# Kernel tuning notes

Hardware: AMD Instinct MI355X
Metric: run time of the kernel (lower is better)

## Reference

```python
import jax, jax.numpy as jnp
import numpy as np

N = 100000   # nodes
M = 50000    # hyperedges
E = 600000   # incidences
D_IN = 128
D_OUT = 128


def setup_inputs() -> dict:
    key = jax.random.key(0)
    ks = jax.random.split(key, 7)
    x = jax.random.normal(ks[0], (N, D_IN), dtype=jnp.float32)
    row = jax.random.randint(ks[1], (E,), 0, N, dtype=jnp.int64)  # node ids
    col = jax.random.randint(ks[2], (E,), 0, M, dtype=jnp.int64)  # hyperedge ids
    edge_index = jnp.stack([row, col], axis=0)
    s_v = 1.0 / np.sqrt(D_IN)
    s_e = 1.0 / np.sqrt(D_OUT)
    s_u = 1.0 / np.sqrt(2 * D_OUT)
    W_v = jax.random.uniform(ks[3], (D_IN, D_OUT), jnp.float32, -s_v, s_v)
    W_e = jax.random.uniform(ks[4], (D_OUT, D_OUT), jnp.float32, -s_e, s_e)
    W_upd = jax.random.uniform(ks[5], (2 * D_OUT, D_OUT), jnp.float32, -s_u, s_u)
    b_upd = jax.random.uniform(ks[6], (D_OUT,), jnp.float32, -s_u, s_u)
    return {"x": x, "edge_index": edge_index, "W_v": W_v, "W_e": W_e,
            "W_upd": W_upd, "b_upd": b_upd}


def _mean_reduce(vals, index, K):
    # vals: (E, D); scatter-mean into (K, D)
    s = jax.ops.segment_sum(vals, index, num_segments=K)
    cnt = jax.ops.segment_sum(jnp.ones((vals.shape[0], 1), vals.dtype), index,
                              num_segments=K)
    return s / jnp.maximum(cnt, 1.0)


def reference(x, edge_index, W_v, W_e, W_upd, b_upd):
    row, col = edge_index[0], edge_index[1]
    x_self = x @ W_v                                # (N, D)
    # vertex -> hyperedge (mean pooling)
    e_feat = _mean_reduce(x_self[row], col, M)      # (M, D)
    e_proj = e_feat @ W_e                           # (M, D)
    # hyperedge -> vertex (mean pooling)
    n_agg = _mean_reduce(e_proj[col], row, N)       # (N, D)
    out = jnp.concatenate([x_self, n_agg], axis=-1) # (N, 2D)
    return jax.nn.relu(out @ W_upd + b_upd)
```

## Files before the change

kernel.cpp:

```cpp
#include <hip/hip_runtime.h>

typedef unsigned short u16;
typedef unsigned int u32;
typedef __attribute__((ext_vector_type(8))) short bf16x8;
typedef __attribute__((ext_vector_type(4))) float f32x4;

__device__ inline u16 f2bf(float f) {
    u32 u = __float_as_uint(f);
    return (u16)((u + 0x7FFFu + ((u >> 16) & 1u)) >> 16);
}
__device__ inline bf16x8 pack8(float4 a, float4 b) {
    bf16x8 v = { (short)f2bf(a.x), (short)f2bf(a.y), (short)f2bf(a.z), (short)f2bf(a.w),
                 (short)f2bf(b.x), (short)f2bf(b.y), (short)f2bf(b.z), (short)f2bf(b.w) };
    return v;
}
__device__ inline float bflo(u32 v) { return __uint_as_float(v << 16); }
__device__ inline float bfhi(u32 v) { return __uint_as_float(v & 0xFFFF0000u); }

#define LDA 136
#define CAPE 64
#define CAPN 48
#define PE   6250
#define PN   12500

__device__ inline void gemm128_nolds(
    const float* __restrict__ A, const float* __restrict__ B, int tile,
    u16* __restrict__ Wt, int koff, float* __restrict__ Cf32)
{
    const int tid = threadIdx.x;
    const int col = tid & 127;
    const int rh  = tid >> 7;
    const int r0  = tile * 16;
    float acc[8] = {0.f,0.f,0.f,0.f,0.f,0.f,0.f,0.f};
    for (int k = 0; k < 128; ++k) {
        float bv = B[(size_t)k * 128 + col];
        #pragma unroll
        for (int i = 0; i < 8; ++i)
            acc[i] = fmaf(A[(size_t)(r0 + rh * 8 + i) * 128 + k], bv, acc[i]);
    }
    #pragma unroll
    for (int i = 0; i < 8; ++i) {
        int r = r0 + rh * 8 + i;
        if (Wt)   Wt[(size_t)col * 256 + koff + r] = f2bf(acc[i]);
        if (Cf32) Cf32[(size_t)r * 128 + col] = acc[i];
    }
}

__global__ __launch_bounds__(256) void fill_conv(
    const int* __restrict__ row, const int* __restrict__ col,
    int* __restrict__ cnt_e, int* __restrict__ cnt_n,
    int* __restrict__ adj_e, u16* __restrict__ adj_n, int E,
    const float* __restrict__ x, u16* __restrict__ xb, size_t n8, int nbConv,
    const float* __restrict__ W_v, const float* __restrict__ W_e,
    const float* __restrict__ W_upd, float* __restrict__ T,
    u16* __restrict__ Wt)
{
    u32 bid = blockIdx.x;
    if (bid < 16) {
        if (bid < 8) gemm128_nolds(W_v, W_upd, bid, Wt, 0, nullptr);
        else         gemm128_nolds(W_e, W_upd + 128 * 128, bid - 8, nullptr, 0, T);
        return;
    }
    bid -= 16;
    if (bid < (u32)nbConv) {
        size_t i = (size_t)bid * 256 + threadIdx.x;
        if (i < n8) {
            const float4* s = (const float4*)(x + i * 8);
            *(bf16x8*)(xb + i * 8) = pack8(s[0], s[1]);
        }
        return;
    }
    bid -= nbConv;
    const int chunk = bid >> 3;
    const int part  = bid & 7;
    const int e = chunk * 256 + threadIdx.x;
    if (e >= E) return;
    const int r = row[e], c = col[e];
    if ((u32)c / PE == (u32)part) {
        int pe = atomicAdd(&cnt_e[c], 1);
        if (pe < CAPE) adj_e[(size_t)c * CAPE + pe] = r;
    }
    if ((u32)r / PN == (u32)part) {
        int pn = atomicAdd(&cnt_n[r], 1);
        if (pn < CAPN) adj_n[(size_t)r * CAPN + pn] = (u16)c;
    }
}

template<typename IDX, int CAP>
__device__ inline void gather2_body(
    const u32* __restrict__ src, const IDX* __restrict__ adj,
    const int* __restrict__ cnt, u32* __restrict__ out, int K, int rowBase)
{
    const int tid = threadIdx.x;
    const int row = rowBase + ((tid >> 6) << 1) + ((tid & 63) >> 5);
    const int l32 = tid & 31;
    if (row >= K) return;
    int d = cnt[row];
    if (d > CAP) d = CAP;
    const IDX* a = adj + (size_t)row * CAP;
    float sA0=0.f,sA1=0.f,sA2=0.f,sA3=0.f;
    float sB0=0.f,sB1=0.f,sB2=0.f,sB3=0.f;
    int k = 0;
    for (; k + 4 <= d; k += 4) {
        uint2 v0 = *(const uint2*)(src + (size_t)(u32)a[k]     * 64 + l32 * 2);
        uint2 v1 = *(const uint2*)(src + (size_t)(u32)a[k + 1] * 64 + l32 * 2);
        uint2 v2 = *(const uint2*)(src + (size_t)(u32)a[k + 2] * 64 + l32 * 2);
        uint2 v3 = *(const uint2*)(src + (size_t)(u32)a[k + 3] * 64 + l32 * 2);
        sA0 += bflo(v0.x); sA1 += bfhi(v0.x); sA2 += bflo(v0.y); sA3 += bfhi(v0.y);
        sB0 += bflo(v1.x); sB1 += bfhi(v1.x); sB2 += bflo(v1.y); sB3 += bfhi(v1.y);
        sA0 += bflo(v2.x); sA1 += bfhi(v2.x); sA2 += bflo(v2.y); sA3 += bfhi(v2.y);
        sB0 += bflo(v3.x); sB1 += bfhi(v3.x); sB2 += bflo(v3.y); sB3 += bfhi(v3.y);
    }
    for (; k < d; ++k) {
        uint2 v = *(const uint2*)(src + (size_t)(u32)a[k] * 64 + l32 * 2);
        sA0 += bflo(v.x); sA1 += bfhi(v.x); sA2 += bflo(v.y); sA3 += bfhi(v.y);
    }
    float inv = 1.f / fmaxf((float)d, 1.f);
    float s0 = (sA0 + sB0) * inv, s1 = (sA1 + sB1) * inv;
    float s2 = (sA2 + sB2) * inv, s3 = (sA3 + sB3) * inv;
    uint2 res;
    res.x = ((u32)f2bf(s1) << 16) | (u32)f2bf(s0);
    res.y = ((u32)f2bf(s3) << 16) | (u32)f2bf(s2);
    *(uint2*)(out + (size_t)row * 64 + l32 * 2) = res;
}

__global__ __launch_bounds__(256) void gather_e_k(
    const u32* __restrict__ src, const int* __restrict__ adj,
    const int* __restrict__ cnt, u32* __restrict__ out, int K,
    const float* __restrict__ W_v, const float* __restrict__ T,
    u16* __restrict__ Wt)
{
    if (blockIdx.x < 8) {
        gemm128_nolds(W_v, T, blockIdx.x, Wt, 128, nullptr);
        return;
    }
    gather2_body<int, CAPE>(src, adj, cnt, out, K, (blockIdx.x - 8) * 8);
}

__global__ __launch_bounds__(256) void gather_n_k(
    const u32* __restrict__ src, const u16* __restrict__ adj,
    const int* __restrict__ cnt, u32* __restrict__ out, int K)
{
    gather2_body<u16, CAPN>(src, adj, cnt, out, K, blockIdx.x * 8);
}

__global__ __launch_bounds__(256) void mfma_gemm_final(
    const u16* __restrict__ Xbf, const u16* __restrict__ Nbf,
    const u16* __restrict__ Wt, const float* __restrict__ bias,
    float* __restrict__ C, int nrows)
{
    __shared__ u16 Ash[64 * LDA];
    __shared__ u16 Bsh[128 * LDA];
    const int tid = threadIdx.x;
    const int r0 = blockIdx.x * 64;
    const int w = tid >> 6, lane = tid & 63;
    const int lr = lane & 15, lk = (lane >> 4) << 3;

    f32x4 acc[8] = { {0,0,0,0},{0,0,0,0},{0,0,0,0},{0,0,0,0},
                     {0,0,0,0},{0,0,0,0},{0,0,0,0},{0,0,0,0} };

    for (int ph = 0; ph < 2; ++ph) {
        __syncthreads();
        const u16* Asrc = ph ? Nbf : Xbf;
        #pragma unroll
        for (int p = 0; p < 4; ++p) {
            int chunk = p * 256 + tid;
            int r = chunk >> 4, cg = (chunk & 15) << 3;
            int gr = r0 + r;
            bf16x8 v = {0,0,0,0,0,0,0,0};
            if (gr < nrows)
                v = *(const bf16x8*)(Asrc + (size_t)gr * 128 + cg);
            *(bf16x8*)&Ash[r * LDA + cg] = v;
        }
        #pragma unroll
        for (int p = 0; p < 8; ++p) {
            int chunk = p * 256 + tid;
            int n = chunk >> 4, kg = (chunk & 15) << 3;
            *(bf16x8*)&Bsh[n * LDA + kg] =
                *(const bf16x8*)(Wt + (size_t)n * 256 + ph * 128 + kg);
        }
        __syncthreads();
        #pragma unroll
        for (int ks = 0; ks < 4; ++ks) {
            bf16x8 af = *(bf16x8*)&Ash[(w * 16 + lr) * LDA + ks * 32 + lk];
            #pragma unroll
            for (int t = 0; t < 8; ++t) {
                bf16x8 bfr = *(bf16x8*)&Bsh[(t * 16 + lr) * LDA + ks * 32 + lk];
                acc[t] = __builtin_amdgcn_mfma_f32_16x16x32_bf16(af, bfr, acc[t], 0, 0, 0);
            }
        }
    }

    const int rbase = r0 + w * 16 + ((lane >> 4) << 2);
    #pragma unroll
    for (int t = 0; t < 8; ++t) {
        int gc = t * 16 + lr;
        float bv = bias[gc];
        #pragma unroll
        for (int reg = 0; reg < 4; ++reg) {
            int gr = rbase + reg;
            if (gr < nrows) C[(size_t)gr * 128 + gc] = fmaxf(acc[t][reg] + bv, 0.f);
        }
    }
}

extern "C" void kernel_launch(void* const* d_in, const int* in_sizes, int n_in,
                              void* d_out, int out_size, void* d_ws, size_t ws_size,
                              hipStream_t stream)
{
    const float* x     = (const float*)d_in[0];
    const int*   ei    = (const int*)  d_in[1];
    const float* W_v   = (const float*)d_in[2];
    const float* W_e   = (const float*)d_in[3];
    const float* W_upd = (const float*)d_in[4];
    const float* b_upd = (const float*)d_in[5];

    const int N = in_sizes[0] / 128;
    const int E = in_sizes[1] / 2;
    const int M = 50000;

    const int* row = ei;
    const int* col = ei + E;

    char* p = (char*)d_ws;
    u16* x_bf   = (u16*)p;  p += (size_t)N * 128 * 2;
    u16* xbar   = (u16*)p;  p += (size_t)M * 128 * 2;
    u16* nbar   = (u16*)p;  p += (size_t)N * 128 * 2;
    float* T    = (float*)p; p += 128 * 128 * 4;
    u16* Wt     = (u16*)p;  p += 128 * 256 * 2;
    int* cnt_e  = (int*)p;  p += (size_t)M * 4;
    int* cnt_n  = (int*)p;  p += (size_t)N * 4;
    int* adj_e  = (int*)p;  p += (size_t)M * CAPE * 4;
    u16* adj_n  = (u16*)p;  p += (size_t)N * CAPN * 2;

    const int nchunks = (E + 255) / 256;
    const int nbFill8 = nchunks * 8;
    const size_t n8 = (size_t)N * 128 / 8;
    const int nbConv = (int)((n8 + 255) / 256);

    hipMemsetAsync(cnt_e, 0, (size_t)(M + N) * sizeof(int), stream);

    fill_conv<<<16 + nbConv + nbFill8, 256, 0, stream>>>(
        row, col, cnt_e, cnt_n, adj_e, adj_n, E,
        x, x_bf, n8, nbConv, W_v, W_e, W_upd, T, Wt);

    gather_e_k<<<8 + (M + 7) / 8, 256, 0, stream>>>(
        (const u32*)x_bf, adj_e, cnt_e, (u32*)xbar, M, W_v, T, Wt);

    gather_n_k<<<(N + 7) / 8, 256, 0, stream>>>(
        (const u32*)xbar, adj_n, cnt_n, (u32*)nbar, N);

    mfma_gemm_final<<<(N + 63) / 64, 256, 0, stream>>>(
        x_bf, nbar, Wt, b_upd, (float*)d_out, N);
}
```

Measured before the change: 159.6 us.

## Widen gather loads, drop LDS staging in final GEMM, reorder fill blocks

```diff
diff --git a/kernel.cpp b/kernel.cpp
--- a/kernel.cpp
+++ b/kernel.cpp
@@ -17,7 +17,6 @@
 __device__ inline float bflo(u32 v) { return __uint_as_float(v << 16); }
 __device__ inline float bfhi(u32 v) { return __uint_as_float(v & 0xFFFF0000u); }
 
-#define LDA 136
 #define CAPE 64
 #define CAPN 48
 #define PE   6250
@@ -49,8 +48,8 @@
 __global__ __launch_bounds__(256) void fill_conv(
     const int* __restrict__ row, const int* __restrict__ col,
     int* __restrict__ cnt_e, int* __restrict__ cnt_n,
-    int* __restrict__ adj_e, u16* __restrict__ adj_n, int E,
-    const float* __restrict__ x, u16* __restrict__ xb, size_t n8, int nbConv,
+    int* __restrict__ adj_e, u16* __restrict__ adj_n, int E, int nbFill8,
+    const float* __restrict__ x, u16* __restrict__ xb, size_t n8,
     const float* __restrict__ W_v, const float* __restrict__ W_e,
     const float* __restrict__ W_upd, float* __restrict__ T,
     u16* __restrict__ Wt)
@@ -62,66 +61,73 @@
         return;
     }
     bid -= 16;
-    if (bid < (u32)nbConv) {
-        size_t i = (size_t)bid * 256 + threadIdx.x;
-        if (i < n8) {
-            const float4* s = (const float4*)(x + i * 8);
-            *(bf16x8*)(xb + i * 8) = pack8(s[0], s[1]);
+    if (bid < (u32)nbFill8) {
+        const int chunk = bid >> 3;
+        const int part  = bid & 7;
+        const int e = chunk * 256 + threadIdx.x;
+        if (e >= E) return;
+        const int r = row[e], c = col[e];
+        if ((u32)c / PE == (u32)part) {
+            int pe = atomicAdd(&cnt_e[c], 1);
+            if (pe < CAPE) adj_e[(size_t)c * CAPE + pe] = r;
+        }
+        if ((u32)r / PN == (u32)part) {
+            int pn = atomicAdd(&cnt_n[r], 1);
+            if (pn < CAPN) adj_n[(size_t)r * CAPN + pn] = (u16)c;
         }
         return;
     }
-    bid -= nbConv;
-    const int chunk = bid >> 3;
-    const int part  = bid & 7;
-    const int e = chunk * 256 + threadIdx.x;
-    if (e >= E) return;
-    const int r = row[e], c = col[e];
-    if ((u32)c / PE == (u32)part) {
-        int pe = atomicAdd(&cnt_e[c], 1);
-        if (pe < CAPE) adj_e[(size_t)c * CAPE + pe] = r;
-    }
-    if ((u32)r / PN == (u32)part) {
-        int pn = atomicAdd(&cnt_n[r], 1);
-        if (pn < CAPN) adj_n[(size_t)r * CAPN + pn] = (u16)c;
+    bid -= nbFill8;
+    size_t i = (size_t)bid * 256 + threadIdx.x;
+    if (i < n8) {
+        const float4* s = (const float4*)(x + i * 8);
+        *(bf16x8*)(xb + i * 8) = pack8(s[0], s[1]);
     }
 }
 
 template<typename IDX, int CAP>
-__device__ inline void gather2_body(
+__device__ inline void gather4_body(
     const u32* __restrict__ src, const IDX* __restrict__ adj,
     const int* __restrict__ cnt, u32* __restrict__ out, int K, int rowBase)
 {
     const int tid = threadIdx.x;
-    const int row = rowBase + ((tid >> 6) << 1) + ((tid & 63) >> 5);
-    const int l32 = tid & 31;
+    const int row = rowBase + (tid >> 4);
+    const int l16 = tid & 15;
     if (row >= K) return;
     int d = cnt[row];
     if (d > CAP) d = CAP;
     const IDX* a = adj + (size_t)row * CAP;
-    float sA0=0.f,sA1=0.f,sA2=0.f,sA3=0.f;
-    float sB0=0.f,sB1=0.f,sB2=0.f,sB3=0.f;
+    float a0=0,a1=0,a2=0,a3=0,a4=0,a5=0,a6=0,a7=0;
+    float b0=0,b1=0,b2=0,b3=0,b4=0,b5=0,b6=0,b7=0;
     int k = 0;
     for (; k + 4 <= d; k += 4) {
-        uint2 v0 = *(const uint2*)(src + (size_t)(u32)a[k]     * 64 + l32 * 2);
-        uint2 v1 = *(const uint2*)(src + (size_t)(u32)a[k + 1] * 64 + l32 * 2);
-        uint2 v2 = *(const uint2*)(src + (size_t)(u32)a[k + 2] * 64 + l32 * 2);
-        uint2 v3 = *(const uint2*)(src + (size_t)(u32)a[k + 3] * 64 + l32 * 2);
-        sA0 += bflo(v0.x); sA1 += bfhi(v0.x); sA2 += bflo(v0.y); sA3 += bfhi(v0.y);
-        sB0 += bflo(v1.x); sB1 += bfhi(v1.x); sB2 += bflo(v1.y); sB3 += bfhi(v1.y);
-        sA0 += bflo(v2.x); sA1 += bfhi(v2.x); sA2 += bflo(v2.y); sA3 += bfhi(v2.y);
-        sB0 += bflo(v3.x); sB1 += bfhi(v3.x); sB2 += bflo(v3.y); sB3 += bfhi(v3.y);
+        uint4 v0 = *(const uint4*)(src + (size_t)(u32)a[k]     * 64 + l16 * 4);
+        uint4 v1 = *(const uint4*)(src + (size_t)(u32)a[k + 1] * 64 + l16 * 4);
+        uint4 v2 = *(const uint4*)(src + (size_t)(u32)a[k + 2] * 64 + l16 * 4);
+        uint4 v3 = *(const uint4*)(src + (size_t)(u32)a[k + 3] * 64 + l16 * 4);
+        a0+=bflo(v0.x); a1+=bfhi(v0.x); a2+=bflo(v0.y); a3+=bfhi(v0.y);
+        a4+=bflo(v0.z); a5+=bfhi(v0.z); a6+=bflo(v0.w); a7+=bfhi(v0.w);
+        b0+=bflo(v1.x); b1+=bfhi(v1.x); b2+=bflo(v1.y); b3+=bfhi(v1.y);
+        b4+=bflo(v1.z); b5+=bfhi(v1.z); b6+=bflo(v1.w); b7+=bfhi(v1.w);
+        a0+=bflo(v2.x); a1+=bfhi(v2.x); a2+=bflo(v2.y); a3+=bfhi(v2.y);
+        a4+=bflo(v2.z); a5+=bfhi(v2.z); a6+=bflo(v2.w); a7+=bfhi(v2.w);
+        b0+=bflo(v3.x); b1+=bfhi(v3.x); b2+=bflo(v3.y); b3+=bfhi(v3.y);
+        b4+=bflo(v3.z); b5+=bfhi(v3.z); b6+=bflo(v3.w); b7+=bfhi(v3.w);
     }
     for (; k < d; ++k) {
-        uint2 v = *(const uint2*)(src + (size_t)(u32)a[k] * 64 + l32 * 2);
-        sA0 += bflo(v.x); sA1 += bfhi(v.x); sA2 += bflo(v.y); sA3 += bfhi(v.y);
+        uint4 v = *(const uint4*)(src + (size_t)(u32)a[k] * 64 + l16 * 4);
+        a0+=bflo(v.x); a1+=bfhi(v.x); a2+=bflo(v.y); a3+=bfhi(v.y);
+        a4+=bflo(v.z); a5+=bfhi(v.z); a6+=bflo(v.w); a7+=bfhi(v.w);
     }
     float inv = 1.f / fmaxf((float)d, 1.f);
-    float s0 = (sA0 + sB0) * inv, s1 = (sA1 + sB1) * inv;
-    float s2 = (sA2 + sB2) * inv, s3 = (sA3 + sB3) * inv;
-    uint2 res;
+    float s0=(a0+b0)*inv, s1=(a1+b1)*inv, s2=(a2+b2)*inv, s3=(a3+b3)*inv;
+    float s4=(a4+b4)*inv, s5=(a5+b5)*inv, s6=(a6+b6)*inv, s7=(a7+b7)*inv;
+    uint4 res;
     res.x = ((u32)f2bf(s1) << 16) | (u32)f2bf(s0);
     res.y = ((u32)f2bf(s3) << 16) | (u32)f2bf(s2);
-    *(uint2*)(out + (size_t)row * 64 + l32 * 2) = res;
+    res.z = ((u32)f2bf(s5) << 16) | (u32)f2bf(s4);
+    res.w = ((u32)f2bf(s7) << 16) | (u32)f2bf(s6);
+    *(uint4*)(out + (size_t)row * 64 + l16 * 4) = res;
 }
 
 __global__ __launch_bounds__(256) void gather_e_k(
@@ -134,14 +140,14 @@
         gemm128_nolds(W_v, T, blockIdx.x, Wt, 128, nullptr);
         return;
     }
-    gather2_body<int, CAPE>(src, adj, cnt, out, K, (blockIdx.x - 8) * 8);
+    gather4_body<int, CAPE>(src, adj, cnt, out, K, (blockIdx.x - 8) * 16);
 }
 
 __global__ __launch_bounds__(256) void gather_n_k(
     const u32* __restrict__ src, const u16* __restrict__ adj,
     const int* __restrict__ cnt, u32* __restrict__ out, int K)
 {
-    gather2_body<u16, CAPN>(src, adj, cnt, out, K, blockIdx.x * 8);
+    gather4_body<u16, CAPN>(src, adj, cnt, out, K, blockIdx.x * 16);
 }
 
 __global__ __launch_bounds__(256) void mfma_gemm_final(
@@ -149,43 +155,27 @@
     const u16* __restrict__ Wt, const float* __restrict__ bias,
     float* __restrict__ C, int nrows)
 {
-    __shared__ u16 Ash[64 * LDA];
-    __shared__ u16 Bsh[128 * LDA];
     const int tid = threadIdx.x;
     const int r0 = blockIdx.x * 64;
     const int w = tid >> 6, lane = tid & 63;
     const int lr = lane & 15, lk = (lane >> 4) << 3;
+    const int arow = r0 + w * 16 + lr;
 
     f32x4 acc[8] = { {0,0,0,0},{0,0,0,0},{0,0,0,0},{0,0,0,0},
                      {0,0,0,0},{0,0,0,0},{0,0,0,0},{0,0,0,0} };
 
+    #pragma unroll
     for (int ph = 0; ph < 2; ++ph) {
-        __syncthreads();
         const u16* Asrc = ph ? Nbf : Xbf;
         #pragma unroll
-        for (int p = 0; p < 4; ++p) {
-            int chunk = p * 256 + tid;
-            int r = chunk >> 4, cg = (chunk & 15) << 3;
-            int gr = r0 + r;
-            bf16x8 v = {0,0,0,0,0,0,0,0};
-            if (gr < nrows)
-                v = *(const bf16x8*)(Asrc + (size_t)gr * 128 + cg);
-            *(bf16x8*)&Ash[r * LDA + cg] = v;
-        }
-        #pragma unroll
-        for (int p = 0; p < 8; ++p) {
-            int chunk = p * 256 + tid;
-            int n = chunk >> 4, kg = (chunk & 15) << 3;
-            *(bf16x8*)&Bsh[n * LDA + kg] =
-                *(const bf16x8*)(Wt + (size_t)n * 256 + ph * 128 + kg);
-        }
-        __syncthreads();
-        #pragma unroll
         for (int ks = 0; ks < 4; ++ks) {
-            bf16x8 af = *(bf16x8*)&Ash[(w * 16 + lr) * LDA + ks * 32 + lk];
+            bf16x8 af = {0,0,0,0,0,0,0,0};
+            if (arow < nrows)
+                af = *(const bf16x8*)(Asrc + (size_t)arow * 128 + ks * 32 + lk);
             #pragma unroll
             for (int t = 0; t < 8; ++t) {
-                bf16x8 bfr = *(bf16x8*)&Bsh[(t * 16 + lr) * LDA + ks * 32 + lk];
+                bf16x8 bfr = *(const bf16x8*)(
+                    Wt + (size_t)(t * 16 + lr) * 256 + ph * 128 + ks * 32 + lk);
                 acc[t] = __builtin_amdgcn_mfma_f32_16x16x32_bf16(af, bfr, acc[t], 0, 0, 0);
             }
         }
@@ -199,7 +189,9 @@
         #pragma unroll
         for (int reg = 0; reg < 4; ++reg) {
             int gr = rbase + reg;
-            if (gr < nrows) C[(size_t)gr * 128 + gc] = fmaxf(acc[t][reg] + bv, 0.f);
+            if (gr < nrows)
+                __builtin_nontemporal_store(fmaxf(acc[t][reg] + bv, 0.f),
+                                            C + (size_t)gr * 128 + gc);
         }
     }
 }
@@ -240,14 +232,14 @@
 
     hipMemsetAsync(cnt_e, 0, (size_t)(M + N) * sizeof(int), stream);
 
-    fill_conv<<<16 + nbConv + nbFill8, 256, 0, stream>>>(
-        row, col, cnt_e, cnt_n, adj_e, adj_n, E,
-        x, x_bf, n8, nbConv, W_v, W_e, W_upd, T, Wt);
-
-    gather_e_k<<<8 + (M + 7) / 8, 256, 0, stream>>>(
+    fill_conv<<<16 + nbFill8 + nbConv, 256, 0, stream>>>(
+        row, col, cnt_e, cnt_n, adj_e, adj_n, E, nbFill8,
+        x, x_bf, n8, W_v, W_e, W_upd, T, Wt);
+
+    gather_e_k<<<8 + (M + 15) / 16, 256, 0, stream>>>(
         (const u32*)x_bf, adj_e, cnt_e, (u32*)xbar, M, W_v, T, Wt);
 
-    gather_n_k<<<(N + 7) / 8, 256, 0, stream>>>(
+    gather_n_k<<<(N + 15) / 16, 256, 0, stream>>>(
         (const u32*)xbar, adj_n, cnt_n, (u32*)nbar, N);
 
     mfma_gemm_final<<<(N + 63) / 64, 256, 0, stream>>>(
```

After: 195.4 us. 22.5% more time.
